# Optimization experiments

Hardware: AMD Instinct MI355X
Metric: run time of the kernel (lower is better)

The kernel has to match this reference:

```python
import jax, jax.numpy as jnp
import numpy as np

MARGIN = 1.0
B, D, NUM_CLASSES = 8192, 128, 10


def setup_inputs() -> dict:
    key = jax.random.key(0)
    k1, k2 = jax.random.split(key)
    embeddings = jax.random.normal(k1, (B, D), dtype=jnp.float32)
    labels = jax.random.randint(k2, (B,), 0, NUM_CLASSES, dtype=jnp.int64)
    return {"embeddings": embeddings, "labels": labels}


def reference(embeddings, labels):
    # pairwise Euclidean distances d[i, j] = sqrt(sum((e_i - e_j)^2))
    sq = jnp.sum(embeddings * embeddings, axis=-1)               # [B]
    d2 = sq[:, None] + sq[None, :] - 2.0 * (embeddings @ embeddings.T)
    dist = jnp.sqrt(jnp.maximum(d2, 0.0))                        # [B, B]

    same = labels[:, None] == labels[None, :]                    # [B, B] bool
    neg_inf = jnp.float32(-jnp.inf)
    pos_inf = jnp.float32(jnp.inf)

    # hardest positive: max distance among same-class (includes self, dist 0, harmless)
    hardest_pos = jnp.max(jnp.where(same, dist, neg_inf), axis=1)   # [B]
    # hardest negative: min distance among different-class
    hardest_neg = jnp.min(jnp.where(same, pos_inf, dist), axis=1)   # [B]

    per_anchor = jax.nn.relu(hardest_pos - hardest_neg + MARGIN)    # [B]
    # use_gt_than_zero_mean=False -> divide by batch size
    return jnp.sum(per_anchor) / per_anchor.shape[0]
```

## Files before the change

### kernel.cpp

```cpp
#include <hip/hip_runtime.h>
#include <hip/hip_bf16.h>
#include <cstdint>

#define BATCH 8192
#define DIM   128
#define MARGIN 1.0f

typedef __attribute__((ext_vector_type(8))) short short8;
typedef __attribute__((ext_vector_type(4))) float f32x4;
typedef __attribute__((ext_vector_type(4))) int   i32x4;

__device__ __forceinline__ void async_copy16(const __hip_bfloat16* g, unsigned short* lds) {
    __builtin_amdgcn_global_load_lds(
        (const __attribute__((address_space(1))) unsigned int*)g,
        (__attribute__((address_space(3))) unsigned int*)lds, 16, 0, 0);
}

__global__ __launch_bounds__(256) void bhtl_prep(
    const float* __restrict__ emb,
    __hip_bfloat16* __restrict__ Ebf,
    float* __restrict__ sq,
    unsigned* __restrict__ hp2,
    unsigned* __restrict__ hn2)
{
    const int w   = threadIdx.x >> 6;
    const int l   = threadIdx.x & 63;
    const int row = blockIdx.x * 4 + w;
    const float2 e = ((const float2*)(emb + row * DIM))[l];
    __hip_bfloat162 h2;
    h2.x = __float2bfloat16(e.x);
    h2.y = __float2bfloat16(e.y);
    ((__hip_bfloat162*)(Ebf + row * DIM))[l] = h2;
    float s = e.x * e.x + e.y * e.y;
    #pragma unroll
    for (int d = 1; d < 64; d <<= 1) s += __shfl_xor(s, d, 64);
    if (l == 0) {
        sq[row]  = s;
        hp2[row] = 0u;
        hn2[row] = 0x7F800000u;
    }
}

__global__ __launch_bounds__(256) void bhtl_main(
    const __hip_bfloat16* __restrict__ Ebf,
    const float* __restrict__ sq,
    const int* __restrict__ labels,
    unsigned* __restrict__ hp2,
    unsigned* __restrict__ hn2)
{
    __shared__ __align__(16) unsigned short B_s[2][16384];

    const int tid  = threadIdx.x;
    const int w    = tid >> 6;
    const int lane = tid & 63;
    const int q    = lane >> 4;
    const int ln   = lane & 15;
    const int rt   = blockIdx.x >> 3;
    const int js   = blockIdx.x & 7;
    const int rowbase = rt * 128 + w * 32;
    const int jbase0  = js * 1024;

    const int ubase = w * 512 + lane;
    auto stage = [&](int buf, int chunk) {
        const int jb = jbase0 + chunk * 128;
        #pragma unroll
        for (int c = 0; c < 8; ++c) {
            int U   = ubase + c * 64;
            int col = U >> 4;
            int u   = U & 15;
            int j   = u ^ (col & 7);
            async_copy16(Ebf + (size_t)(jb + col) * DIM + j * 8,
                         &B_s[buf][(w * 512 + c * 64) * 8]);
        }
    };

    short8 af[2][4];
    float  sqi[2];
    int    labi[2];
    #pragma unroll
    for (int m = 0; m < 2; ++m) {
        const int row = rowbase + m * 16 + ln;
        #pragma unroll
        for (int kc = 0; kc < 4; ++kc)
            af[m][kc] = *(const short8*)(Ebf + (size_t)row * DIM + kc * 32 + q * 8);
        sqi[m]  = sq[row];
        labi[m] = labels[row];
    }

    float mp[2] = {-INFINITY, -INFINITY};
    float mn[2] = { INFINITY,  INFINITY};

    stage(0, 0);
    __syncthreads();

    #pragma unroll 2
    for (int ch = 0; ch < 8; ++ch) {
        const int buf = ch & 1;
        if (ch < 7) stage(buf ^ 1, ch + 1);

        const int jb = jbase0 + ch * 128;
        #pragma unroll
        for (int n = 0; n < 8; ++n) {
            short8 bfr[4];
            #pragma unroll
            for (int kc = 0; kc < 4; ++kc)
                bfr[kc] = *(const short8*)(
                    &B_s[buf][(n * 16 + ln) * 128 + (((kc * 4 + q) ^ (ln & 7)) << 3)]);
            f32x4 sqj  = *(const f32x4*)(sq     + jb + n * 16 + q * 4);
            i32x4 labj = *(const i32x4*)(labels + jb + n * 16 + q * 4);

            f32x4 acc[2];
            const f32x4 zero = {0.f, 0.f, 0.f, 0.f};
            acc[0] = zero; acc[1] = zero;
            #pragma unroll
            for (int kc = 0; kc < 4; ++kc)
                #pragma unroll
                for (int m = 0; m < 2; ++m)
                    acc[m] = __builtin_amdgcn_mfma_f32_16x16x32_bf16(
                        bfr[kc], af[m][kc], acc[m], 0, 0, 0);

            #pragma unroll
            for (int m = 0; m < 2; ++m)
                #pragma unroll
                for (int r = 0; r < 4; ++r) {
                    float val = fmaf(-2.0f, acc[m][r], sqj[r]);
                    bool same = (labi[m] == labj[r]);
                    mp[m] = fmaxf(mp[m], same ? val : -INFINITY);
                    mn[m] = fminf(mn[m], same ? INFINITY : val);
                }
        }
        __syncthreads();
    }

    #pragma unroll
    for (int m = 0; m < 2; ++m) {
        float a = mp[m], b = mn[m];
        a = fmaxf(a, __shfl_xor(a, 16, 64));
        a = fmaxf(a, __shfl_xor(a, 32, 64));
        b = fminf(b, __shfl_xor(b, 16, 64));
        b = fminf(b, __shfl_xor(b, 32, 64));
        if (q == 0) {
            const int row = rowbase + m * 16 + ln;
            atomicMax(&hp2[row], __float_as_uint(fmaxf(sqi[m] + a, 0.0f)));
            atomicMin(&hn2[row], __float_as_uint(fmaxf(sqi[m] + b, 0.0f)));
        }
    }
}

__global__ __launch_bounds__(1024) void bhtl_final(
    const unsigned* __restrict__ hp2,
    const unsigned* __restrict__ hn2,
    float* __restrict__ out)
{
    __shared__ float red[16];
    float sum = 0.f;
    for (int i = threadIdx.x; i < BATCH; i += 1024) {
        float hp = sqrtf(__uint_as_float(hp2[i]));
        float hn = sqrtf(__uint_as_float(hn2[i]));
        sum += fmaxf(hp - hn + MARGIN, 0.f);
    }
    #pragma unroll
    for (int d = 1; d < 64; d <<= 1) sum += __shfl_xor(sum, d, 64);
    int wv = threadIdx.x >> 6;
    if ((threadIdx.x & 63) == 0) red[wv] = sum;
    __syncthreads();
    if (threadIdx.x < 64) {
        float v = (threadIdx.x < 16) ? red[threadIdx.x] : 0.f;
        #pragma unroll
        for (int d = 1; d < 16; d <<= 1) v += __shfl_xor(v, d, 64);
        if (threadIdx.x == 0) out[0] = v / (float)BATCH;
    }
}

extern "C" void kernel_launch(void* const* d_in, const int* in_sizes, int n_in,
                              void* d_out, int out_size, void* d_ws, size_t ws_size,
                              hipStream_t stream)
{
    const float* emb    = (const float*)d_in[0];
    const int*   labels = (const int*)d_in[1];
    float*       out    = (float*)d_out;

    char* ws = (char*)d_ws;
    __hip_bfloat16* Ebf = (__hip_bfloat16*)ws;
    float*    sq   = (float*)   (ws + 2 * 1024 * 1024);
    unsigned* hp2  = (unsigned*)(ws + 2 * 1024 * 1024 + 32 * 1024);
    unsigned* hn2  = (unsigned*)(ws + 2 * 1024 * 1024 + 64 * 1024);

    bhtl_prep<<<BATCH / 4, 256, 0, stream>>>(emb, Ebf, sq, hp2, hn2);
    bhtl_main<<<512, 256, 0, stream>>>(Ebf, sq, labels, hp2, hn2);
    bhtl_final<<<1, 1024, 0, stream>>>(hp2, hn2, out);
}
```

Baseline: 89.05 us.

## Give each wave a private LDS pipeline with larger row tile and no block barriers

The main kernel moves from 4-wave blocks sharing a B tile to 2-wave blocks where each wave stages its own 32-column B chunks into private LDS and computes a 64-row by 32-column tile per step. Block-wide __syncthreads are replaced by per-wave vmcnt waits. The column norms and labels are prefetched into LDS once instead of being read from global memory every step. This raises per-wave MFMA reuse of the A fragments and removes cross-wave synchronization, at the cost of more registers per wave, duplicated B loads across waves, and reliance on wave-local ordering of the async LDS copies.

```diff
diff --git a/kernel.cpp b/kernel.cpp
--- a/kernel.cpp
+++ b/kernel.cpp
@@ -10,7 +10,7 @@
 typedef __attribute__((ext_vector_type(4))) float f32x4;
 typedef __attribute__((ext_vector_type(4))) int   i32x4;
 
-__device__ __forceinline__ void async_copy16(const __hip_bfloat16* g, unsigned short* lds) {
+__device__ __forceinline__ void async_copy16(const void* g, void* lds) {
     __builtin_amdgcn_global_load_lds(
         (const __attribute__((address_space(1))) unsigned int*)g,
         (__attribute__((address_space(3))) unsigned int*)lds, 16, 0, 0);
@@ -41,44 +41,52 @@
     }
 }
 
-__global__ __launch_bounds__(256) void bhtl_main(
+__global__ __launch_bounds__(128) void bhtl_main(
     const __hip_bfloat16* __restrict__ Ebf,
     const float* __restrict__ sq,
     const int* __restrict__ labels,
     unsigned* __restrict__ hp2,
     unsigned* __restrict__ hn2)
 {
-    __shared__ __align__(16) unsigned short B_s[2][16384];
+    __shared__ __align__(16) unsigned short B_s[2][2][4096];
+    __shared__ __align__(16) float sqm[2][512];
+    __shared__ __align__(16) int   labm[2][512];
 
     const int tid  = threadIdx.x;
     const int w    = tid >> 6;
     const int lane = tid & 63;
     const int q    = lane >> 4;
     const int ln   = lane & 15;
-    const int rt   = blockIdx.x >> 3;
-    const int js   = blockIdx.x & 7;
-    const int rowbase = rt * 128 + w * 32;
-    const int jbase0  = js * 1024;
-
-    const int ubase = w * 512 + lane;
-    auto stage = [&](int buf, int chunk) {
-        const int jb = jbase0 + chunk * 128;
+    const int rt   = blockIdx.x >> 4;
+    const int js   = blockIdx.x & 15;
+    const int rowbase = rt * 128 + w * 64;
+    const int jbase   = js * 512;
+
+    #pragma unroll
+    for (int c = 0; c < 2; ++c) {
+        int U = c * 64 + lane;
+        async_copy16(sq     + jbase + U * 4, &sqm [w][c * 256]);
+        async_copy16(labels + jbase + U * 4, &labm[w][c * 256]);
+    }
+
+    auto stageB = [&](int buf, int ch) {
+        const int jb = jbase + ch * 32;
         #pragma unroll
         for (int c = 0; c < 8; ++c) {
-            int U   = ubase + c * 64;
+            int U   = c * 64 + lane;
             int col = U >> 4;
             int u   = U & 15;
             int j   = u ^ (col & 7);
             async_copy16(Ebf + (size_t)(jb + col) * DIM + j * 8,
-                         &B_s[buf][(w * 512 + c * 64) * 8]);
+                         &B_s[w][buf][c * 64 * 8]);
         }
     };
 
-    short8 af[2][4];
-    float  sqi[2];
-    int    labi[2];
-    #pragma unroll
-    for (int m = 0; m < 2; ++m) {
+    short8 af[4][4];
+    float  sqi[4];
+    int    labi[4];
+    #pragma unroll
+    for (int m = 0; m < 4; ++m) {
         const int row = rowbase + m * 16 + ln;
         #pragma unroll
         for (int kc = 0; kc < 4; ++kc)
@@ -87,53 +95,64 @@
         labi[m] = labels[row];
     }
 
-    float mp[2] = {-INFINITY, -INFINITY};
-    float mn[2] = { INFINITY,  INFINITY};
-
-    stage(0, 0);
-    __syncthreads();
+    float mp[4] = {-INFINITY, -INFINITY, -INFINITY, -INFINITY};
+    float mn[4] = { INFINITY,  INFINITY,  INFINITY,  INFINITY};
+
+    stageB(0, 0);
 
     #pragma unroll 2
-    for (int ch = 0; ch < 8; ++ch) {
+    for (int ch = 0; ch < 16; ++ch) {
         const int buf = ch & 1;
-        if (ch < 7) stage(buf ^ 1, ch + 1);
-
-        const int jb = jbase0 + ch * 128;
-        #pragma unroll
-        for (int n = 0; n < 8; ++n) {
-            short8 bfr[4];
+
+        asm volatile("s_waitcnt vmcnt(0)" ::: "memory");
+
+        short8 bfr[2][4];
+        #pragma unroll
+        for (int n = 0; n < 2; ++n)
             #pragma unroll
             for (int kc = 0; kc < 4; ++kc)
-                bfr[kc] = *(const short8*)(
-                    &B_s[buf][(n * 16 + ln) * 128 + (((kc * 4 + q) ^ (ln & 7)) << 3)]);
-            f32x4 sqj  = *(const f32x4*)(sq     + jb + n * 16 + q * 4);
-            i32x4 labj = *(const i32x4*)(labels + jb + n * 16 + q * 4);
-
-            f32x4 acc[2];
-            const f32x4 zero = {0.f, 0.f, 0.f, 0.f};
-            acc[0] = zero; acc[1] = zero;
-            #pragma unroll
-            for (int kc = 0; kc < 4; ++kc)
+                bfr[n][kc] = *(const short8*)(
+                    &B_s[w][buf][((n * 16 + ln) * 16 + (((kc * 4 + q) ^ (ln & 7)))) * 8]);
+        f32x4 sqj[2];
+        i32x4 labj[2];
+        #pragma unroll
+        for (int n = 0; n < 2; ++n) {
+            sqj[n]  = *(const f32x4*)(&sqm [w][ch * 32 + n * 16 + q * 4]);
+            labj[n] = *(const i32x4*)(&labm[w][ch * 32 + n * 16 + q * 4]);
+        }
+
+        if (ch < 15) stageB(buf ^ 1, ch + 1);
+
+        f32x4 acc[4][2];
+        const f32x4 zero = {0.f, 0.f, 0.f, 0.f};
+        #pragma unroll
+        for (int m = 0; m < 4; ++m)
+            #pragma unroll
+            for (int n = 0; n < 2; ++n) acc[m][n] = zero;
+        #pragma unroll
+        for (int kc = 0; kc < 4; ++kc)
+            #pragma unroll
+            for (int m = 0; m < 4; ++m)
                 #pragma unroll
-                for (int m = 0; m < 2; ++m)
-                    acc[m] = __builtin_amdgcn_mfma_f32_16x16x32_bf16(
-                        bfr[kc], af[m][kc], acc[m], 0, 0, 0);
-
-            #pragma unroll
-            for (int m = 0; m < 2; ++m)
+                for (int n = 0; n < 2; ++n)
+                    acc[m][n] = __builtin_amdgcn_mfma_f32_16x16x32_bf16(
+                        bfr[n][kc], af[m][kc], acc[m][n], 0, 0, 0);
+
+        #pragma unroll
+        for (int m = 0; m < 4; ++m)
+            #pragma unroll
+            for (int n = 0; n < 2; ++n)
                 #pragma unroll
                 for (int r = 0; r < 4; ++r) {
-                    float val = fmaf(-2.0f, acc[m][r], sqj[r]);
-                    bool same = (labi[m] == labj[r]);
+                    float val = fmaf(-2.0f, acc[m][n][r], sqj[n][r]);
+                    bool same = (labi[m] == labj[n][r]);
                     mp[m] = fmaxf(mp[m], same ? val : -INFINITY);
                     mn[m] = fminf(mn[m], same ? INFINITY : val);
                 }
-        }
-        __syncthreads();
-    }
-
-    #pragma unroll
-    for (int m = 0; m < 2; ++m) {
+    }
+
+    #pragma unroll
+    for (int m = 0; m < 4; ++m) {
         float a = mp[m], b = mn[m];
         a = fmaxf(a, __shfl_xor(a, 16, 64));
         a = fmaxf(a, __shfl_xor(a, 32, 64));
@@ -187,6 +206,6 @@
     unsigned* hn2  = (unsigned*)(ws + 2 * 1024 * 1024 + 64 * 1024);
 
     bhtl_prep<<<BATCH / 4, 256, 0, stream>>>(emb, Ebf, sq, hp2, hn2);
-    bhtl_main<<<512, 256, 0, stream>>>(Ebf, sq, labels, hp2, hn2);
+    bhtl_main<<<1024, 128, 0, stream>>>(Ebf, sq, labels, hp2, hn2);
     bhtl_final<<<1, 1024, 0, stream>>>(hp2, hn2, out);
 }
```

New measurement: 93.68 us. +5.2%, slower.
